# Kernel tuning notes

Measured on AMD Instinct MI355X. Metric: run time of the kernel, lower is better.

## Reference

```python
import jax, jax.numpy as jnp
import numpy as np


def hard_sigmoid(x):
    # Keras hard_sigmoid: clip(0.2*x + 0.5, 0, 1)
    return jnp.clip(0.2 * x + 0.5, 0.0, 1.0)


def setup_inputs() -> dict:
    key = jax.random.key(0)
    k1, k2, k3 = jax.random.split(key, 3)
    B, H, W, C = 32, 64, 64, 256
    x = jax.random.normal(k1, (B, H, W, C), dtype=jnp.float32)
    # glorot_uniform over (C, W, H): fan_in = W (last-two matmul dims are W x H)
    limit = np.sqrt(6.0 / (W + H)).astype(np.float32)
    Wq = jax.random.uniform(k2, (C, W, H), minval=-limit, maxval=limit, dtype=jnp.float32)
    Wk = jax.random.uniform(k3, (C, W, H), minval=-limit, maxval=limit, dtype=jnp.float32)
    return {"x": x, "Wq": Wq, "Wk": Wk}


def reference(x, Wq, Wk):
    # x: [B, H, W, C] -> [B, C, H, W]
    xt = jnp.transpose(x, (0, 3, 1, 2))
    # projections: [B,C,H,W] @ [C,W,H] (broadcast over B) -> [B,C,H,H]
    q = hard_sigmoid(jnp.einsum('bchw,cwk->bchk', xt, Wq))
    K = jnp.tanh(jnp.einsum('bchw,cwk->bchk', xt, Wk))
    # scores: q @ K^T over last two dims -> [B,C,H,H]
    qk = hard_sigmoid(jnp.einsum('bchk,bcmk->bchm', q, K))
    qk = jax.nn.softmax(qk, axis=-1)
    # output: [B,C,H,W] @ [B,C,W(==H),H] -> [B,C,H,H]
    out = jnp.einsum('bchw,bcwm->bchm', xt, qk)
    # back to channels-last [B,H,W,C]
    return jnp.transpose(out, (0, 2, 3, 1))
```

## Files before the change

### kernel.cpp

```cpp
#include <hip/hip_runtime.h>


typedef short short8 __attribute__((ext_vector_type(8)));
typedef float floatx4 __attribute__((ext_vector_type(4)));
typedef unsigned int uint;

__device__ __forceinline__ uint cvtpk(float a, float b) {
  uint r;
  asm("v_cvt_pk_bf16_f32 %0, %1, %2" : "=v"(r) : "v"(a), "v"(b));
  return r;
}
__device__ __forceinline__ short8 u4s8(uint a, uint b, uint c, uint d) {
  union { uint u[4]; short8 s; } t;
  t.u[0] = a; t.u[1] = b; t.u[2] = c; t.u[3] = d;
  return t.s;
}
__device__ __forceinline__ float hsg(float x) {
  return fminf(fmaxf(0.2f * x + 0.5f, 0.f), 1.f);
}

__device__ __forceinline__ void pl32swap(uint A, uint C, uint& lo, uint& hi, int quad) {
#if __has_builtin(__builtin_amdgcn_permlane32_swap)
  auto r = __builtin_amdgcn_permlane32_swap(A, C, false, false);
  lo = (uint)r[0]; hi = (uint)r[1];
#else
  uint sA = __shfl_xor(A, 32), sC = __shfl_xor(C, 32);
  bool up = quad >= 2;
  lo = up ? sC : A;
  hi = up ? C : sA;
#endif
}
__device__ __forceinline__ void pl16swap(uint A, uint C, uint& lo, uint& hi, int quad) {
#if __has_builtin(__builtin_amdgcn_permlane16_swap)
  auto r = __builtin_amdgcn_permlane16_swap(A, C, false, false);
  lo = (uint)r[0]; hi = (uint)r[1];
#else
  uint sA = (uint)__builtin_amdgcn_ds_swizzle((int)A, 0x401F);
  uint sC = (uint)__builtin_amdgcn_ds_swizzle((int)C, 0x401F);
  bool odd = quad & 1;
  lo = odd ? sC : A;
  hi = odd ? C : sA;
#endif
}
__device__ __forceinline__ short8 xchg4(uint A, uint B, uint C, uint D, int quad) {
  uint Ap, Cp, Bp, Dp, t0, t1, t2, t3;
  pl32swap(A, C, Ap, Cp, quad);
  pl32swap(B, D, Bp, Dp, quad);
  pl16swap(Ap, Cp, t0, t2, quad);
  pl16swap(Bp, Dp, t1, t3, quad);
  return u4s8(t0, t1, t2, t3);
}

__global__ __launch_bounds__(256) void prep_w(const float* __restrict__ Wq,
                                              const float* __restrict__ Wk,
                                              unsigned short* __restrict__ ws) {
  __shared__ __align__(16) unsigned char sm[4 * 8704];
  const int tid = threadIdx.x, lane = tid & 63, wid = tid >> 6;
  const int task = blockIdx.x * 4 + wid;
  const int c = task & 255;
  const float* wp = ((task >> 8) ? Wk : Wq) + (size_t)c * 4096;
  unsigned char* buf = sm + wid * 8704;
  const int l15 = lane & 15, quad = lane >> 4;
#pragma unroll 4
  for (int j = 0; j < 16; ++j) {
    int f4 = j * 64 + lane;
    float4 v = *(const float4*)(wp + (size_t)f4 * 4);
    int w = f4 >> 4, k0 = (f4 & 15) << 2;
    uint2 pk; pk.x = cvtpk(v.x, v.y); pk.y = cvtpk(v.z, v.w);
    *(uint2*)(buf + w * 136 + k0 * 2) = pk;
  }
  unsigned short* dst = ws + (size_t)task * 4096;
#pragma unroll
  for (int kt = 0; kt < 4; ++kt)
#pragma unroll
    for (int ks = 0; ks < 2; ++ks) {
      const unsigned short* p = (const unsigned short*)buf + (ks * 32 + quad * 8) * 68 + (kt * 16 + l15);
      short8 af = u4s8((uint)p[0]   | ((uint)p[68]  << 16),
                       (uint)p[136] | ((uint)p[204] << 16),
                       (uint)p[272] | ((uint)p[340] << 16),
                       (uint)p[408] | ((uint)p[476] << 16));
      *(short8*)(dst + ((kt * 2 + ks) * 64 + lane) * 8) = af;
    }
}

__global__ __launch_bounds__(256, 3) void fused_attn(
    const float* __restrict__ x, const unsigned short* __restrict__ wsp,
    float* __restrict__ out) {
  __shared__ __align__(16) unsigned char smem[4 * 8192];

  const int tid  = threadIdx.x;
  const int lane = tid & 63;
  const int wid  = tid >> 6;
  const int l15  = lane & 15;
  const int quad = lane >> 4;

  const int b  = blockIdx.x & 31;
  const int cg = blockIdx.x >> 5;
  const int c0 = cg << 2;
  const int c  = c0 + wid;

  unsigned char* buf0 = smem + wid * 8192;

  const short8* wqf = (const short8*)wsp + (size_t)c * 512;
  const short8* wkf = wqf + 256 * 512;

  short8 aq[4][2];
#pragma unroll
  for (int kt = 0; kt < 4; ++kt)
#pragma unroll
    for (int ks = 0; ks < 2; ++ks) aq[kt][ks] = wqf[(kt * 2 + ks) * 64 + lane];

  {
    const float* xb = x + (size_t)b * 4096 * 256 + c0;
#pragma unroll
    for (int i = 0; i < 8; ++i) {
      int p = i * 256 + tid;
      int h = p >> 5, w0 = (p & 31) << 1;
      const float* src = xb + (size_t)(h * 64 + w0) * 256;
      float4 v0 = *(const float4*)src;
      float4 v1 = *(const float4*)(src + 256);
      uint off = (uint)(h * 128 + (((w0 >> 3) ^ (h & 7)) << 4) + ((w0 & 7) << 1));
      uint pw0 = cvtpk(v0.x, v1.x), pw1 = cvtpk(v0.y, v1.y);
      uint pw2 = cvtpk(v0.z, v1.z), pw3 = cvtpk(v0.w, v1.w);
      *(uint*)(smem + 0 * 8192 + off) = pw0;
      *(uint*)(smem + 1 * 8192 + off) = pw1;
      *(uint*)(smem + 2 * 8192 + off) = pw2;
      *(uint*)(smem + 3 * 8192 + off) = pw3;
    }
  }
  __syncthreads();

  short8 xf[4][2];
#pragma unroll
  for (int rt = 0; rt < 4; ++rt) {
    int r = rt * 16 + l15;
#pragma unroll
    for (int ks = 0; ks < 2; ++ks)
      xf[rt][ks] = *(const short8*)(buf0 + r * 128 + (((ks * 4 + quad) ^ (r & 7)) << 4));
  }

  const floatx4 zero4 = {0.f, 0.f, 0.f, 0.f};
  floatx4 acc[16];

#pragma unroll
  for (int i = 0; i < 16; ++i) acc[i] = zero4;
  __builtin_amdgcn_s_setprio(1);
#pragma unroll
  for (int kt = 0; kt < 4; ++kt)
#pragma unroll
    for (int ht = 0; ht < 4; ++ht) {
      acc[kt * 4 + ht] = __builtin_amdgcn_mfma_f32_16x16x32_bf16(aq[kt][0], xf[ht][0], acc[kt * 4 + ht], 0, 0, 0);
      acc[kt * 4 + ht] = __builtin_amdgcn_mfma_f32_16x16x32_bf16(aq[kt][1], xf[ht][1], acc[kt * 4 + ht], 0, 0, 0);
    }
  __builtin_amdgcn_s_setprio(0);

  short8 qf[4][2];
#pragma unroll
  for (int ht = 0; ht < 4; ++ht) {
    uint s[4][2];
#pragma unroll
    for (int kt = 0; kt < 4; ++kt) {
      floatx4 a = acc[kt * 4 + ht];
      s[kt][0] = cvtpk(hsg(a[0]), hsg(a[1]));
      s[kt][1] = cvtpk(hsg(a[2]), hsg(a[3]));
    }
#pragma unroll
    for (int ks = 0; ks < 2; ++ks)
      qf[ht][ks] = xchg4(s[2 * ks][0], s[2 * ks][1], s[2 * ks + 1][0], s[2 * ks + 1][1], quad);
  }

#pragma unroll
  for (int i = 0; i < 16; ++i) acc[i] = zero4;
#pragma unroll
  for (int kt = 0; kt < 4; ++kt) {
    short8 a0 = wkf[(kt * 2 + 0) * 64 + lane];
    short8 a1 = wkf[(kt * 2 + 1) * 64 + lane];
    __builtin_amdgcn_s_setprio(1);
#pragma unroll
    for (int ht = 0; ht < 4; ++ht) {
      acc[kt * 4 + ht] = __builtin_amdgcn_mfma_f32_16x16x32_bf16(a0, xf[ht][0], acc[kt * 4 + ht], 0, 0, 0);
      acc[kt * 4 + ht] = __builtin_amdgcn_mfma_f32_16x16x32_bf16(a1, xf[ht][1], acc[kt * 4 + ht], 0, 0, 0);
    }
    __builtin_amdgcn_s_setprio(0);
  }
#pragma unroll
  for (int kt = 0; kt < 4; ++kt)
#pragma unroll
    for (int ht = 0; ht < 4; ++ht) {
      floatx4 a = acc[kt * 4 + ht];
      float kv[4];
#pragma unroll
      for (int i = 0; i < 4; ++i) {
        float t = __expf(2.f * a[i]);
        kv[i] = 1.f - 2.f / (t + 1.f);
      }
      uint2 pk; pk.x = cvtpk(kv[0], kv[1]); pk.y = cvtpk(kv[2], kv[3]);
      int m = ht * 16 + l15;
      *(uint2*)(buf0 + m * 128 + ((((kt * 2 + (quad >> 1)) ^ (m & 7))) << 4) + ((quad & 1) << 3)) = pk;
    }

#pragma unroll
  for (int i = 0; i < 16; ++i) acc[i] = zero4;
#pragma unroll
  for (int mt = 0; mt < 4; ++mt) {
    int r = mt * 16 + l15;
    short8 kf0 = *(const short8*)(buf0 + r * 128 + (((quad) ^ (r & 7)) << 4));
    short8 kf1 = *(const short8*)(buf0 + r * 128 + (((4 + quad) ^ (r & 7)) << 4));
    __builtin_amdgcn_s_setprio(1);
#pragma unroll
    for (int wt = 0; wt < 4; ++wt) {
      acc[wt * 4 + mt] = __builtin_amdgcn_mfma_f32_16x16x32_bf16(qf[wt][0], kf0, acc[wt * 4 + mt], 0, 0, 0);
      acc[wt * 4 + mt] = __builtin_amdgcn_mfma_f32_16x16x32_bf16(qf[wt][1], kf1, acc[wt * 4 + mt], 0, 0, 0);
    }
    __builtin_amdgcn_s_setprio(0);
  }
#pragma unroll
  for (int i = 0; i < 16; ++i)
#pragma unroll
    for (int j = 0; j < 4; ++j) acc[i][j] = __expf(hsg(acc[i][j]));
  float inv[4][4];
#pragma unroll
  for (int wt = 0; wt < 4; ++wt)
#pragma unroll
    for (int i = 0; i < 4; ++i) {
      float p = acc[wt * 4 + 0][i] + acc[wt * 4 + 1][i] + acc[wt * 4 + 2][i] + acc[wt * 4 + 3][i];
      p += __shfl_xor(p, 1, 16);
      p += __shfl_xor(p, 2, 16);
      p += __shfl_xor(p, 4, 16);
      p += __shfl_xor(p, 8, 16);
      inv[wt][i] = 1.f / p;
    }
  short8 sf[4][2];
#pragma unroll
  for (int mt = 0; mt < 4; ++mt) {
    uint s[4][2];
#pragma unroll
    for (int wt = 0; wt < 4; ++wt) {
      floatx4 a = acc[wt * 4 + mt];
      s[wt][0] = cvtpk(a[0] * inv[wt][0], a[1] * inv[wt][1]);
      s[wt][1] = cvtpk(a[2] * inv[wt][2], a[3] * inv[wt][3]);
    }
#pragma unroll
    for (int ks = 0; ks < 2; ++ks)
      sf[mt][ks] = xchg4(s[2 * ks][0], s[2 * ks][1], s[2 * ks + 1][0], s[2 * ks + 1][1], quad);
  }

#pragma unroll
  for (int i = 0; i < 16; ++i) acc[i] = zero4;
  __builtin_amdgcn_s_setprio(1);
#pragma unroll
  for (int mt = 0; mt < 4; ++mt)
#pragma unroll
    for (int ht = 0; ht < 4; ++ht) {
      acc[mt * 4 + ht] = __builtin_amdgcn_mfma_f32_16x16x32_bf16(sf[mt][0], xf[ht][0], acc[mt * 4 + ht], 0, 0, 0);
      acc[mt * 4 + ht] = __builtin_amdgcn_mfma_f32_16x16x32_bf16(sf[mt][1], xf[ht][1], acc[mt * 4 + ht], 0, 0, 0);
    }
  __builtin_amdgcn_s_setprio(0);
#pragma unroll
  for (int mt = 0; mt < 4; ++mt)
#pragma unroll
    for (int ht = 0; ht < 4; ++ht) {
      floatx4 a = acc[mt * 4 + ht];
      uint2 pk; pk.x = cvtpk(a[0], a[1]); pk.y = cvtpk(a[2], a[3]);
      int h = ht * 16 + l15;
      *(uint2*)(buf0 + h * 128 + ((((mt * 2 + (quad >> 1)) ^ (h & 7))) << 4) + ((quad & 1) << 3)) = pk;
    }
  __syncthreads();

  const size_t outbase = (size_t)b * 4096 * 256 + c0;
#pragma unroll
  for (int rep = 0; rep < 4; ++rep) {
    int idx = rep * 256 + tid;
    int h = idx >> 4, mq = idx & 15;
    uint loff = (uint)(h * 128 + ((((mq >> 1) ^ (h & 7))) << 4) + ((mq & 1) << 3));
    float vals[4][4];
#pragma unroll
    for (int j = 0; j < 4; ++j) {
      uint2 d = *(const uint2*)(smem + j * 8192 + loff);
      vals[j][0] = __uint_as_float(d.x << 16);
      vals[j][1] = __uint_as_float(d.x & 0xFFFF0000u);
      vals[j][2] = __uint_as_float(d.y << 16);
      vals[j][3] = __uint_as_float(d.y & 0xFFFF0000u);
    }
    float* op = out + outbase + (size_t)(h * 64 + mq * 4) * 256;
#pragma unroll
    for (int jj = 0; jj < 4; ++jj) {
      float4 v = {vals[0][jj], vals[1][jj], vals[2][jj], vals[3][jj]};
      *(float4*)(op + (size_t)jj * 256) = v;
    }
  }
}

extern "C" void kernel_launch(void* const* d_in, const int* in_sizes, int n_in,
                              void* d_out, int out_size, void* d_ws, size_t ws_size,
                              hipStream_t stream) {
  const float* x  = (const float*)d_in[0];
  const float* Wq = (const float*)d_in[1];
  const float* Wk = (const float*)d_in[2];
  unsigned short* ws = (unsigned short*)d_ws;
  prep_w<<<dim3(128), dim3(256), 0, stream>>>(Wq, Wk, ws);
  fused_attn<<<dim3(2048), dim3(256), 0, stream>>>(x, ws, (float*)d_out);
}
```

Before: 332.8 us.

## Remap blocks to XCDs, batch x loads, keep K in registers, prefetch Wk

Remaps the block index so that each of the 8 XCDs handles a contiguous range of channel groups across all batches, aiming for better L2 locality of weights and x. The x staging loads are grouped into batches of four before any conversion, to raise memory-level parallelism. The Wk fragments are software-prefetched two k-tiles ahead. The tanh(K) result is turned into MFMA operands through a register lane exchange instead of a round trip through LDS. The x fragments are re-read from LDS just before the final matmul, which shortens their register live range at the cost of extra LDS reads.

```diff
diff --git a/kernel.cpp b/kernel.cpp
--- a/kernel.cpp
+++ b/kernel.cpp
@@ -94,10 +94,14 @@
   const int l15  = lane & 15;
   const int quad = lane >> 4;
 
-  const int b  = blockIdx.x & 31;
-  const int cg = blockIdx.x >> 5;
-  const int c0 = cg << 2;
-  const int c  = c0 + wid;
+  const int p    = blockIdx.x;
+  const int xcd  = p & 7;
+  const int slot = p >> 3;
+  const int cg4  = xcd * 2 + (slot >> 7);
+  const int b    = (slot >> 2) & 31;
+  const int cg   = (cg4 << 2) + (slot & 3);
+  const int c0   = cg << 2;
+  const int c    = c0 + wid;
 
   unsigned char* buf0 = smem + wid * 8192;
 
@@ -113,19 +117,26 @@
   {
     const float* xb = x + (size_t)b * 4096 * 256 + c0;
 #pragma unroll
-    for (int i = 0; i < 8; ++i) {
-      int p = i * 256 + tid;
-      int h = p >> 5, w0 = (p & 31) << 1;
-      const float* src = xb + (size_t)(h * 64 + w0) * 256;
-      float4 v0 = *(const float4*)src;
-      float4 v1 = *(const float4*)(src + 256);
-      uint off = (uint)(h * 128 + (((w0 >> 3) ^ (h & 7)) << 4) + ((w0 & 7) << 1));
-      uint pw0 = cvtpk(v0.x, v1.x), pw1 = cvtpk(v0.y, v1.y);
-      uint pw2 = cvtpk(v0.z, v1.z), pw3 = cvtpk(v0.w, v1.w);
-      *(uint*)(smem + 0 * 8192 + off) = pw0;
-      *(uint*)(smem + 1 * 8192 + off) = pw1;
-      *(uint*)(smem + 2 * 8192 + off) = pw2;
-      *(uint*)(smem + 3 * 8192 + off) = pw3;
+    for (int bat = 0; bat < 2; ++bat) {
+      float4 va[4], vb[4];
+#pragma unroll
+      for (int i = 0; i < 4; ++i) {
+        int p4 = (bat * 4 + i) * 256 + tid;
+        int h = p4 >> 5, w0 = (p4 & 31) << 1;
+        const float* src = xb + (size_t)(h * 64 + w0) * 256;
+        va[i] = *(const float4*)src;
+        vb[i] = *(const float4*)(src + 256);
+      }
+#pragma unroll
+      for (int i = 0; i < 4; ++i) {
+        int p4 = (bat * 4 + i) * 256 + tid;
+        int h = p4 >> 5, w0 = (p4 & 31) << 1;
+        uint off = (uint)(h * 128 + (((w0 >> 3) ^ (h & 7)) << 4) + ((w0 & 7) << 1));
+        *(uint*)(smem + 0 * 8192 + off) = cvtpk(va[i].x, vb[i].x);
+        *(uint*)(smem + 1 * 8192 + off) = cvtpk(va[i].y, vb[i].y);
+        *(uint*)(smem + 2 * 8192 + off) = cvtpk(va[i].z, vb[i].z);
+        *(uint*)(smem + 3 * 8192 + off) = cvtpk(va[i].w, vb[i].w);
+      }
     }
   }
   __syncthreads();
@@ -138,6 +149,10 @@
     for (int ks = 0; ks < 2; ++ks)
       xf[rt][ks] = *(const short8*)(buf0 + r * 128 + (((ks * 4 + quad) ^ (r & 7)) << 4));
   }
+
+  short8 wkp[2][2];
+  wkp[0][0] = wkf[0 * 64 + lane]; wkp[0][1] = wkf[1 * 64 + lane];
+  wkp[1][0] = wkf[2 * 64 + lane]; wkp[1][1] = wkf[3 * 64 + lane];
 
   const floatx4 zero4 = {0.f, 0.f, 0.f, 0.f};
   floatx4 acc[16];
@@ -173,8 +188,11 @@
   for (int i = 0; i < 16; ++i) acc[i] = zero4;
 #pragma unroll
   for (int kt = 0; kt < 4; ++kt) {
-    short8 a0 = wkf[(kt * 2 + 0) * 64 + lane];
-    short8 a1 = wkf[(kt * 2 + 1) * 64 + lane];
+    short8 a0 = wkp[kt & 1][0], a1 = wkp[kt & 1][1];
+    if (kt < 2) {
+      wkp[kt & 1][0] = wkf[((kt + 2) * 2 + 0) * 64 + lane];
+      wkp[kt & 1][1] = wkf[((kt + 2) * 2 + 1) * 64 + lane];
+    }
     __builtin_amdgcn_s_setprio(1);
 #pragma unroll
     for (int ht = 0; ht < 4; ++ht) {
@@ -183,37 +201,39 @@
     }
     __builtin_amdgcn_s_setprio(0);
   }
-#pragma unroll
-  for (int kt = 0; kt < 4; ++kt)
-#pragma unroll
-    for (int ht = 0; ht < 4; ++ht) {
+  short8 kf[4][2];
+#pragma unroll
+  for (int ht = 0; ht < 4; ++ht) {
+    uint t[4][2];
+#pragma unroll
+    for (int kt = 0; kt < 4; ++kt) {
       floatx4 a = acc[kt * 4 + ht];
       float kv[4];
 #pragma unroll
       for (int i = 0; i < 4; ++i) {
-        float t = __expf(2.f * a[i]);
-        kv[i] = 1.f - 2.f / (t + 1.f);
+        float e = __expf(2.f * a[i]);
+        kv[i] = 1.f - 2.f / (e + 1.f);
       }
-      uint2 pk; pk.x = cvtpk(kv[0], kv[1]); pk.y = cvtpk(kv[2], kv[3]);
-      int m = ht * 16 + l15;
-      *(uint2*)(buf0 + m * 128 + ((((kt * 2 + (quad >> 1)) ^ (m & 7))) << 4) + ((quad & 1) << 3)) = pk;
-    }
+      t[kt][0] = cvtpk(kv[0], kv[1]);
+      t[kt][1] = cvtpk(kv[2], kv[3]);
+    }
+#pragma unroll
+    for (int ks = 0; ks < 2; ++ks)
+      kf[ht][ks] = xchg4(t[2 * ks][0], t[2 * ks][1], t[2 * ks + 1][0], t[2 * ks + 1][1], quad);
+  }
 
 #pragma unroll
   for (int i = 0; i < 16; ++i) acc[i] = zero4;
-#pragma unroll
-  for (int mt = 0; mt < 4; ++mt) {
-    int r = mt * 16 + l15;
-    short8 kf0 = *(const short8*)(buf0 + r * 128 + (((quad) ^ (r & 7)) << 4));
-    short8 kf1 = *(const short8*)(buf0 + r * 128 + (((4 + quad) ^ (r & 7)) << 4));
-    __builtin_amdgcn_s_setprio(1);
+  __builtin_amdgcn_s_setprio(1);
+#pragma unroll
+  for (int mt = 0; mt < 4; ++mt)
 #pragma unroll
     for (int wt = 0; wt < 4; ++wt) {
-      acc[wt * 4 + mt] = __builtin_amdgcn_mfma_f32_16x16x32_bf16(qf[wt][0], kf0, acc[wt * 4 + mt], 0, 0, 0);
-      acc[wt * 4 + mt] = __builtin_amdgcn_mfma_f32_16x16x32_bf16(qf[wt][1], kf1, acc[wt * 4 + mt], 0, 0, 0);
-    }
-    __builtin_amdgcn_s_setprio(0);
-  }
+      acc[wt * 4 + mt] = __builtin_amdgcn_mfma_f32_16x16x32_bf16(qf[wt][0], kf[mt][0], acc[wt * 4 + mt], 0, 0, 0);
+      acc[wt * 4 + mt] = __builtin_amdgcn_mfma_f32_16x16x32_bf16(qf[wt][1], kf[mt][1], acc[wt * 4 + mt], 0, 0, 0);
+    }
+  __builtin_amdgcn_s_setprio(0);
+
 #pragma unroll
   for (int i = 0; i < 16; ++i)
 #pragma unroll
@@ -223,12 +243,12 @@
   for (int wt = 0; wt < 4; ++wt)
 #pragma unroll
     for (int i = 0; i < 4; ++i) {
-      float p = acc[wt * 4 + 0][i] + acc[wt * 4 + 1][i] + acc[wt * 4 + 2][i] + acc[wt * 4 + 3][i];
-      p += __shfl_xor(p, 1, 16);
-      p += __shfl_xor(p, 2, 16);
-      p += __shfl_xor(p, 4, 16);
-      p += __shfl_xor(p, 8, 16);
-      inv[wt][i] = 1.f / p;
+      float pp = acc[wt * 4 + 0][i] + acc[wt * 4 + 1][i] + acc[wt * 4 + 2][i] + acc[wt * 4 + 3][i];
+      pp += __shfl_xor(pp, 1, 16);
+      pp += __shfl_xor(pp, 2, 16);
+      pp += __shfl_xor(pp, 4, 16);
+      pp += __shfl_xor(pp, 8, 16);
+      inv[wt][i] = 1.f / pp;
     }
   short8 sf[4][2];
 #pragma unroll
@@ -245,6 +265,14 @@
       sf[mt][ks] = xchg4(s[2 * ks][0], s[2 * ks][1], s[2 * ks + 1][0], s[2 * ks + 1][1], quad);
   }
 
+  short8 xg[4][2];
+#pragma unroll
+  for (int rt = 0; rt < 4; ++rt) {
+    int r = rt * 16 + l15;
+#pragma unroll
+    for (int ks = 0; ks < 2; ++ks)
+      xg[rt][ks] = *(const short8*)(buf0 + r * 128 + (((ks * 4 + quad) ^ (r & 7)) << 4));
+  }
 #pragma unroll
   for (int i = 0; i < 16; ++i) acc[i] = zero4;
   __builtin_amdgcn_s_setprio(1);
@@ -252,8 +280,8 @@
   for (int mt = 0; mt < 4; ++mt)
 #pragma unroll
     for (int ht = 0; ht < 4; ++ht) {
-      acc[mt * 4 + ht] = __builtin_amdgcn_mfma_f32_16x16x32_bf16(sf[mt][0], xf[ht][0], acc[mt * 4 + ht], 0, 0, 0);
-      acc[mt * 4 + ht] = __builtin_amdgcn_mfma_f32_16x16x32_bf16(sf[mt][1], xf[ht][1], acc[mt * 4 + ht], 0, 0, 0);
+      acc[mt * 4 + ht] = __builtin_amdgcn_mfma_f32_16x16x32_bf16(sf[mt][0], xg[ht][0], acc[mt * 4 + ht], 0, 0, 0);
+      acc[mt * 4 + ht] = __builtin_amdgcn_mfma_f32_16x16x32_bf16(sf[mt][1], xg[ht][1], acc[mt * 4 + ht], 0, 0, 0);
     }
   __builtin_amdgcn_s_setprio(0);
 #pragma unroll
```

New measurement: 371.5 us. +11.6%, slower.
